# Performance work log

Measured on AMD Instinct MI355X. Metric: run time of the kernel, lower is better.

## Reference

```python
import jax, jax.numpy as jnp
import numpy as np

DIM = 768
H = 12        # query heads
HKV = 4       # kv heads
G = H // HKV  # GQA group size
HD = 64       # head dim
CAP = 50.0    # soft cap (Gemma-2 style)
EPS = 1e-6
SCALE = HD ** -0.5
B, T, S = 1, 128, 256


def setup_inputs() -> dict:
    key = jax.random.key(0)
    ks = jax.random.split(key, 5)
    s = DIM ** -0.5
    x = jax.random.normal(ks[0], (B, T, S, DIM), jnp.float32)
    Wq = jax.random.normal(ks[1], (DIM, H * HD), jnp.float32) * s
    Wk = jax.random.normal(ks[2], (DIM, HKV * HD), jnp.float32) * s
    Wv = jax.random.normal(ks[3], (DIM, HKV * HD), jnp.float32) * s
    Wo = jax.random.normal(ks[4], (H * HD, DIM), jnp.float32) * s
    q_norm_w = jnp.ones((HD,), jnp.float32)
    k_norm_w = jnp.ones((HD,), jnp.float32)
    return {"x": x, "Wq": Wq, "Wk": Wk, "Wv": Wv, "Wo": Wo,
            "q_norm_w": q_norm_w, "k_norm_w": k_norm_w}


def _rmsnorm(x, w):
    # x: (..., HD)
    return x * jax.lax.rsqrt(jnp.mean(x * x, axis=-1, keepdims=True) + EPS) * w


def reference(x, Wq, Wk, Wv, Wo, q_norm_w, k_norm_w):
    b, t, s, d = x.shape
    n = b * s
    # fold spatial into batch: temporal attention per spatial position
    xf = x.transpose(0, 2, 1, 3).reshape(n, t, d)             # (N, T, D)
    q = (xf @ Wq).reshape(n, t, H, HD).transpose(0, 2, 1, 3)   # (N, H, T, hd)
    k = (xf @ Wk).reshape(n, t, HKV, HD).transpose(0, 2, 1, 3) # (N, Hkv, T, hd)
    v = (xf @ Wv).reshape(n, t, HKV, HD).transpose(0, 2, 1, 3)
    # QKNorm (per-head RMSNorm on head_dim)
    q = _rmsnorm(q, q_norm_w)
    k = _rmsnorm(k, k_norm_w)
    # GQA without materializing repeated K/V: split q heads into (Hkv, G)
    # (repeat_interleave maps query head h -> kv head h // G, matching kv*G+g)
    qg = q.reshape(n, HKV, G, t, HD)
    attn = jnp.einsum('bkgtd,bksd->bkgts', qg, k) * SCALE      # (N, Hkv, G, T, T)
    attn = CAP * jnp.tanh(attn / CAP)                          # soft cap
    causal = jnp.triu(jnp.ones((t, t), bool), 1)               # True above diag
    attn = jnp.where(causal, -jnp.inf, attn)
    attn = jax.nn.softmax(attn, axis=-1)
    out = jnp.einsum('bkgts,bksd->bkgtd', attn, v)             # (N, Hkv, G, T, hd)
    out = out.reshape(n, H, t, HD).transpose(0, 2, 1, 3).reshape(n, t, H * HD)
    out = out @ Wo                                             # (N, T, D)
    return out.reshape(b, s, t, d).transpose(0, 2, 1, 3)        # (B, T, S, D)
```

## Files before the change

### kernel.cpp

```cpp
#include <hip/hip_runtime.h>
#include <stdint.h>
#include <stddef.h>

#define DIM 768
#define NH  12
#define NKV 4
#define HD  64
#define TT  128
#define NS  256

typedef __attribute__((ext_vector_type(8))) short bf16x8;
typedef __attribute__((ext_vector_type(4))) float f32x4;
typedef __attribute__((ext_vector_type(4))) unsigned int u32x4;
typedef __attribute__((ext_vector_type(2))) unsigned int u32x2;

__device__ __forceinline__ unsigned short f2bf(float f) {
  union { float f; unsigned int u; } v; v.f = f;
  return (unsigned short)((v.u + 0x7FFFu + ((v.u >> 16) & 1u)) >> 16);
}

__device__ __forceinline__ void gload_lds16(const void* g, void* l) {
  __builtin_amdgcn_global_load_lds(
      (const __attribute__((address_space(1))) unsigned int*)g,
      (__attribute__((address_space(3))) unsigned int*)l, 16, 0, 0);
}

__global__ __launch_bounds__(256)
void prep_kernel(const float* __restrict__ x, const float* __restrict__ Wq,
                 const float* __restrict__ Wk, const float* __restrict__ Wv,
                 const float* __restrict__ Wo, unsigned short* __restrict__ Wt,
                 unsigned short* __restrict__ WoT, unsigned short* __restrict__ xb) {
  const int b = blockIdx.x, tid = threadIdx.x;
  if (b < 6144) {
    int idx = b * 256 + tid;
    const int n1 = 1280 * DIM;
    if (idx < n1) {
      int c = idx / DIM, kk = idx - c * DIM;
      float v;
      if (c < 768)       v = Wq[kk * 768 + c];
      else if (c < 1024) v = Wk[kk * 256 + (c - 768)];
      else               v = Wv[kk * 256 + (c - 1024)];
      Wt[idx] = f2bf(v);
    } else {
      int i2 = idx - n1;
      int c = i2 / DIM, kk = i2 - c * DIM;
      WoT[i2] = f2bf(Wo[kk * 768 + c]);
    }
  } else {
    int g = (b - 6144) * 256 + tid;
    int r = g / 192;
    int k = g - r * 192;
    int t = r >> 8, n = r & 255;
    f32x4 f = *reinterpret_cast<const f32x4*>(x + (size_t)g * 4);
    u32x2 pk;
    pk[0] = (unsigned)f2bf(f[0]) | ((unsigned)f2bf(f[1]) << 16);
    pk[1] = (unsigned)f2bf(f[2]) | ((unsigned)f2bf(f[3]) << 16);
    *reinterpret_cast<u32x2*>(xb + (size_t)((n << 7) + t) * DIM + k * 4) = pk;
  }
}


#define STAGE256(bufp, ko)                                                       \
  { unsigned short* Ad = lds + (bufp) * 32768;                                   \
    unsigned short* Bd = Ad + 16384;                                             \
    gload_lds16(a0src + (size_t)(wave * 8) * DIM + (ko), Ad + (wave * 8) * 64);  \
    gload_lds16(a0src + (size_t)(64 + wave * 8) * DIM + (ko), Ad + (64 + wave * 8) * 64); \
    gload_lds16(a1src + (size_t)(wave * 8) * DIM + (ko), Ad + (128 + wave * 8) * 64);     \
    gload_lds16(a1src + (size_t)(64 + wave * 8) * DIM + (ko), Ad + (192 + wave * 8) * 64);\
    gload_lds16(bsrc + (size_t)(wave * 8) * DIM + (ko), Bd + (wave * 8) * 64);   \
    gload_lds16(bsrc + (size_t)(64 + wave * 8) * DIM + (ko), Bd + (64 + wave * 8) * 64);  \
    gload_lds16(bsrc + (size_t)(128 + wave * 8) * DIM + (ko), Bd + (128 + wave * 8) * 64);\
    gload_lds16(bsrc + (size_t)(192 + wave * 8) * DIM + (ko), Bd + (192 + wave * 8) * 64); }

#define KLOOP256                                                                 \
  STAGE256(0, 0);                                                                \
  __syncthreads();                                                               \
  for (int kt = 0; kt < 12; ++kt) {                                              \
    if (kt < 11) STAGE256((kt + 1) & 1, (kt + 1) * 64);                          \
    const char* Ab = (const char*)(lds + (kt & 1) * 32768);                      \
    const char* Bb = Ab + 32768;                                                 \
    _Pragma("unroll")                                                            \
    for (int ks = 0; ks < 2; ++ks) {                                             \
      bf16x8 a[8], bbf[4];                                                       \
      _Pragma("unroll")                                                          \
      for (int m = 0; m < 8; ++m)                                                \
        a[m] = *(const bf16x8*)(Ab + (wmw * 128 + m * 16 + cl) * 128 + ((ks * 64 + rowg * 16) ^ swzr)); \
      _Pragma("unroll")                                                          \
      for (int nn = 0; nn < 4; ++nn)                                             \
        bbf[nn] = *(const bf16x8*)(Bb + (wn * 64 + nn * 16 + cl) * 128 + ((ks * 64 + rowg * 16) ^ swzr)); \
      __builtin_amdgcn_s_setprio(1);                                             \
      _Pragma("unroll")                                                          \
      for (int m = 0; m < 8; ++m)                                                \
        _Pragma("unroll")                                                        \
        for (int nn = 0; nn < 4; ++nn)                                           \
          acc[m][nn] = __builtin_amdgcn_mfma_f32_16x16x32_bf16(a[m], bbf[nn], acc[m][nn], 0, 0, 0); \
      __builtin_amdgcn_s_setprio(0);                                             \
    }                                                                            \
    __syncthreads();                                                             \
  }

__global__ __launch_bounds__(512, 2)
void qkv_kernel(const unsigned short* __restrict__ xb, const float* __restrict__ qnw,
                const float* __restrict__ knw, const unsigned short* __restrict__ Wt,
                unsigned short* __restrict__ qb, unsigned short* __restrict__ kb,
                unsigned short* __restrict__ vTb) {
  extern __shared__ unsigned short lds[];
  const int b = blockIdx.x;
  const int x8 = b & 7, idx = b >> 3;
  const int cbt = idx % 5;
  const int np  = (idx / 5) * 8 + x8;
  const int n0  = np * 2;
  const int tid = threadIdx.x;
  const int wave = tid >> 6, lane = tid & 63;
  const int cl = lane & 15, rowg = lane >> 4;
  const int wmw = wave >> 2, wn = wave & 3;
  const int l8 = lane >> 3, s8 = lane & 7;
  const int segs = (s8 ^ l8) * 8;
  const unsigned short* a0src = xb + (size_t)(n0 * TT + l8) * DIM + segs;
  const unsigned short* a1src = xb + (size_t)((n0 + 1) * TT + l8) * DIM + segs;
  const unsigned short* bsrc  = Wt + (size_t)(cbt * 256 + l8) * DIM + segs;
  const int swzr = (cl & 7) << 4;
  f32x4 acc[8][4] = {};

  KLOOP256;

  __syncthreads();
  const int n = n0 + wmw;

  if (cbt == 4) {
    unsigned short* dst = vTb + (size_t)((n * NKV + wn) * HD) * TT;
    #pragma unroll
    for (int m = 0; m < 8; ++m) {
      const int tb = m * 16 + rowg * 4;
      #pragma unroll
      for (int nn = 0; nn < 4; ++nn) {
        const int d = nn * 16 + cl;
        u32x2 pk;
        pk[0] = (unsigned)f2bf(acc[m][nn][0]) | ((unsigned)f2bf(acc[m][nn][1]) << 16);
        pk[1] = (unsigned)f2bf(acc[m][nn][2]) | ((unsigned)f2bf(acc[m][nn][3]) << 16);
        *reinterpret_cast<u32x2*>(dst + (size_t)d * TT + tb) = pk;
      }
    }
  } else {
    const int isq = (cbt < 3);
    const float* nw = isq ? qnw : knw;
    float wfrag[4];
    #pragma unroll
    for (int nn = 0; nn < 4; ++nn) wfrag[nn] = nw[nn * 16 + cl];
    const float rs = isq ? 0.125f : 1.0f;
    unsigned short* slab = lds + (wmw * 4 + wn) * 8192;
    #pragma unroll
    for (int m = 0; m < 8; ++m) {
      #pragma unroll
      for (int j = 0; j < 4; ++j) {
        const int t = m * 16 + rowg * 4 + j;
        float ss = 0.f;
        #pragma unroll
        for (int nn = 0; nn < 4; ++nn) { float v = acc[m][nn][j]; ss += v * v; }
        #pragma unroll
        for (int dlt = 1; dlt < 16; dlt <<= 1) ss += __shfl_xor(ss, dlt);
        const float r = rsqrtf(ss * (1.f / 64.f) + 1e-6f) * rs;
        #pragma unroll
        for (int nn = 0; nn < 4; ++nn)
          slab[t * 64 + nn * 16 + cl] = f2bf(acc[m][nn][j] * r * wfrag[nn]);
      }
    }
    __syncthreads();
    #pragma unroll
    for (int i = 0; i < 16; ++i) {
      const int c = tid + 512 * i;
      const int s = c >> 10, within = c & 1023;
      const int nn2 = n0 + (s >> 2);
      size_t off;
      if (isq) off = ((size_t)nn2 * NH + cbt * 4 + (s & 3)) * TT * HD;
      else     off = ((size_t)nn2 * NKV + (s & 3)) * TT * HD;
      unsigned short* gdst = (isq ? qb : kb) + off + within * 8;
      *reinterpret_cast<u32x4*>(gdst) =
          *reinterpret_cast<const u32x4*>(lds + (size_t)s * 8192 + within * 8);
    }
  }
}

__global__ __launch_bounds__(256)
void attn_kernel(const unsigned short* __restrict__ qb, const unsigned short* __restrict__ kb,
                 const unsigned short* __restrict__ vTb, unsigned short* __restrict__ ab) {
  extern __shared__ char smem[];
  unsigned short (*Ks)[72]   = reinterpret_cast<unsigned short (*)[72]>(smem);
  unsigned short (*Vts)[136] = reinterpret_cast<unsigned short (*)[136]>(smem + 18432);
  unsigned short (*Pl)[136]  = reinterpret_cast<unsigned short (*)[136]>(smem + 35840);
  const int b = blockIdx.x;
  const int x8 = b & 7, idx = b >> 3;
  const int kv = idx & 3;
  const int n  = (idx >> 2) * 8 + x8;
  const int tid = threadIdx.x, wave = tid >> 6, lane = tid & 63;
  const int cl = lane & 15, rowg = lane >> 4;

  const unsigned short* ksrc = kb + (size_t)(n * NKV + kv) * TT * HD;
  const unsigned short* vsrc = vTb + (size_t)(n * NKV + kv) * HD * TT;
  #pragma unroll
  for (int i = 0; i < 4; ++i) {
    int c = tid + 256 * i, r = c >> 3, seg = c & 7;
    *reinterpret_cast<u32x4*>(&Ks[r][seg * 8]) = *reinterpret_cast<const u32x4*>(ksrc + c * 8);
  }
  #pragma unroll
  for (int i = 0; i < 4; ++i) {
    int c = tid + 256 * i, r = c >> 4, seg = c & 15;
    *reinterpret_cast<u32x4*>(&Vts[r][seg * 8]) = *reinterpret_cast<const u32x4*>(vsrc + c * 8);
  }
  __syncthreads();

  for (int hh = 0; hh < 3; ++hh) {
    const int h = kv * 3 + hh;
    const unsigned short* qsrc = qb + (size_t)(n * NH + h) * TT * HD;
    f32x4 sc[2][8] = {};
    #pragma unroll
    for (int ks = 0; ks < 2; ++ks) {
      bf16x8 a[2], bbf[8];
      #pragma unroll
      for (int m = 0; m < 2; ++m)
        a[m] = *reinterpret_cast<const bf16x8*>(
            qsrc + (size_t)(wave * 32 + m * 16 + cl) * HD + ks * 32 + rowg * 8);
      #pragma unroll
      for (int nn = 0; nn < 8; ++nn)
        bbf[nn] = *reinterpret_cast<const bf16x8*>(&Ks[nn * 16 + cl][ks * 32 + rowg * 8]);
      #pragma unroll
      for (int m = 0; m < 2; ++m)
        #pragma unroll
        for (int nn = 0; nn < 8; ++nn)
          sc[m][nn] = __builtin_amdgcn_mfma_f32_16x16x32_bf16(a[m], bbf[nn], sc[m][nn], 0, 0, 0);
    }
    #pragma unroll
    for (int m = 0; m < 2; ++m) {
      #pragma unroll
      for (int j = 0; j < 4; ++j) {
        const int rowv = wave * 32 + m * 16 + rowg * 4 + j;
        float mx = -__builtin_inff();
        #pragma unroll
        for (int nn = 0; nn < 8; ++nn) {
          float s = sc[m][nn][j];
          float e = __expf(s * 0.04f);
          s = 50.f - 100.f * __builtin_amdgcn_rcpf(e + 1.f);
          if (nn * 16 + cl > rowv) s = -__builtin_inff();
          sc[m][nn][j] = s;
          mx = fmaxf(mx, s);
        }
        #pragma unroll
        for (int d = 1; d < 16; d <<= 1) mx = fmaxf(mx, __shfl_xor(mx, d));
        float sum = 0.f;
        #pragma unroll
        for (int nn = 0; nn < 8; ++nn) {
          float e = __expf(sc[m][nn][j] - mx);
          sc[m][nn][j] = e;
          sum += e;
        }
        #pragma unroll
        for (int d = 1; d < 16; d <<= 1) sum += __shfl_xor(sum, d);
        const float inv = __builtin_amdgcn_rcpf(sum);
        #pragma unroll
        for (int nn = 0; nn < 8; ++nn)
          Pl[rowv][nn * 16 + cl] = f2bf(sc[m][nn][j] * inv);
      }
    }
    __syncthreads();
    f32x4 o[2][4] = {};
    #pragma unroll
    for (int ks = 0; ks < 4; ++ks) {
      bf16x8 a[2], bbf[4];
      #pragma unroll
      for (int m = 0; m < 2; ++m)
        a[m] = *reinterpret_cast<const bf16x8*>(&Pl[wave * 32 + m * 16 + cl][ks * 32 + rowg * 8]);
      #pragma unroll
      for (int nn = 0; nn < 4; ++nn)
        bbf[nn] = *reinterpret_cast<const bf16x8*>(&Vts[nn * 16 + cl][ks * 32 + rowg * 8]);
      #pragma unroll
      for (int m = 0; m < 2; ++m)
        #pragma unroll
        for (int nn = 0; nn < 4; ++nn)
          o[m][nn] = __builtin_amdgcn_mfma_f32_16x16x32_bf16(a[m], bbf[nn], o[m][nn], 0, 0, 0);
    }
    unsigned short* dst = ab + (size_t)n * TT * DIM + h * HD;
    #pragma unroll
    for (int m = 0; m < 2; ++m)
      #pragma unroll
      for (int j = 0; j < 4; ++j) {
        int t = wave * 32 + m * 16 + rowg * 4 + j;
        #pragma unroll
        for (int nn = 0; nn < 4; ++nn)
          dst[(size_t)t * DIM + nn * 16 + cl] = f2bf(o[m][nn][j]);
      }
    __syncthreads();
  }
}

__global__ __launch_bounds__(512, 2)
void out_kernel(const unsigned short* __restrict__ ab, const unsigned short* __restrict__ WoT,
                float* __restrict__ out) {
  extern __shared__ unsigned short lds[];
  const int b = blockIdx.x;
  const int x8 = b & 7, idx = b >> 3;
  const int cbt = idx % 3;
  const int np  = (idx / 3) * 8 + x8;
  const int n0  = np * 2;
  const int tid = threadIdx.x;
  const int wave = tid >> 6, lane = tid & 63;
  const int cl = lane & 15, rowg = lane >> 4;
  const int wmw = wave >> 2, wn = wave & 3;
  const int l8 = lane >> 3, s8 = lane & 7;
  const int segs = (s8 ^ l8) * 8;
  const unsigned short* a0src = ab + (size_t)(n0 * TT + l8) * DIM + segs;
  const unsigned short* a1src = ab + (size_t)((n0 + 1) * TT + l8) * DIM + segs;
  const unsigned short* bsrc  = WoT + (size_t)(cbt * 256 + l8) * DIM + segs;
  const int swzr = (cl & 7) << 4;
  f32x4 acc[8][4] = {};

  KLOOP256;

  const int n = n0 + wmw;
  #pragma unroll
  for (int m = 0; m < 8; ++m)
    #pragma unroll
    for (int j = 0; j < 4; ++j) {
      const int t = m * 16 + rowg * 4 + j;
      #pragma unroll
      for (int nn = 0; nn < 4; ++nn)
        out[(size_t)(t * NS + n) * DIM + cbt * 256 + wn * 64 + nn * 16 + cl] = acc[m][nn][j];
    }
}

extern "C" void kernel_launch(void* const* d_in, const int* in_sizes, int n_in,
                              void* d_out, int out_size, void* d_ws, size_t ws_size,
                              hipStream_t stream) {
  const float* x   = (const float*)d_in[0];
  const float* Wq  = (const float*)d_in[1];
  const float* Wk  = (const float*)d_in[2];
  const float* Wv  = (const float*)d_in[3];
  const float* Wo  = (const float*)d_in[4];
  const float* qnw = (const float*)d_in[5];
  const float* knw = (const float*)d_in[6];
  (void)in_sizes; (void)n_in; (void)out_size;

  char* ws = (char*)d_ws;
  unsigned short* Wt  = (unsigned short*)(ws + 0);
  unsigned short* WoT = (unsigned short*)(ws + 1966080);
  unsigned short* qb  = (unsigned short*)(ws + 3145728);
  unsigned short* kb  = (unsigned short*)(ws + 53477376);
  unsigned short* vTb = (unsigned short*)(ws + 70254592);
  unsigned short* ab  = (unsigned short*)(ws + 87031808);
  unsigned short* xb  = ab;
  if (ws_size < 137363456) return;

  hipFuncSetAttribute(reinterpret_cast<const void*>(qkv_kernel),
                      hipFuncAttributeMaxDynamicSharedMemorySize, 131072);
  hipFuncSetAttribute(reinterpret_cast<const void*>(out_kernel),
                      hipFuncAttributeMaxDynamicSharedMemorySize, 131072);
  hipFuncSetAttribute(reinterpret_cast<const void*>(attn_kernel),
                      hipFuncAttributeMaxDynamicSharedMemorySize, 70656);

  prep_kernel<<<30720, 256, 0, stream>>>(x, Wq, Wk, Wv, Wo, Wt, WoT, xb);
  qkv_kernel<<<640, 512, 131072, stream>>>(xb, qnw, knw, Wt, qb, kb, vTb);
  attn_kernel<<<1024, 256, 70656, stream>>>(qb, kb, vTb, ab);
  out_kernel<<<384, 512, 131072, stream>>>(ab, WoT, (float*)d_out);
}
```

Before: 230.8 us.

## Rework GEMM K-loop into 4-stage, K=32 pipeline with split-phase MFMA scheduling

Replaces the double-buffered K=64 GEMM main loop used by the QKV and output projection kernels with a quad-buffered K=32 loop. Each iteration is split into two phases: A and B tile prefetches two steps ahead are interleaved with LDS reads and MFMA groups, using explicit vmcnt/lgkmcnt waits and raw s_barriers in place of __syncthreads. The LDS swizzle and global-to-LDS load mapping are redesigned for 64-byte rows. The aim is to hide global load latency and cut barrier stalls, at the cost of more barriers per K step and hand-tuned wait counts that must match exactly for correctness.

```diff
diff --git a/kernel.cpp b/kernel.cpp
--- a/kernel.cpp
+++ b/kernel.cpp
@@ -60,43 +60,80 @@
 }
 
 
-#define STAGE256(bufp, ko)                                                       \
-  { unsigned short* Ad = lds + (bufp) * 32768;                                   \
-    unsigned short* Bd = Ad + 16384;                                             \
-    gload_lds16(a0src + (size_t)(wave * 8) * DIM + (ko), Ad + (wave * 8) * 64);  \
-    gload_lds16(a0src + (size_t)(64 + wave * 8) * DIM + (ko), Ad + (64 + wave * 8) * 64); \
-    gload_lds16(a1src + (size_t)(wave * 8) * DIM + (ko), Ad + (128 + wave * 8) * 64);     \
-    gload_lds16(a1src + (size_t)(64 + wave * 8) * DIM + (ko), Ad + (192 + wave * 8) * 64);\
-    gload_lds16(bsrc + (size_t)(wave * 8) * DIM + (ko), Bd + (wave * 8) * 64);   \
-    gload_lds16(bsrc + (size_t)(64 + wave * 8) * DIM + (ko), Bd + (64 + wave * 8) * 64);  \
-    gload_lds16(bsrc + (size_t)(128 + wave * 8) * DIM + (ko), Bd + (128 + wave * 8) * 64);\
-    gload_lds16(bsrc + (size_t)(192 + wave * 8) * DIM + (ko), Bd + (192 + wave * 8) * 64); }
-
-#define KLOOP256                                                                 \
-  STAGE256(0, 0);                                                                \
-  __syncthreads();                                                               \
-  for (int kt = 0; kt < 12; ++kt) {                                              \
-    if (kt < 11) STAGE256((kt + 1) & 1, (kt + 1) * 64);                          \
-    const char* Ab = (const char*)(lds + (kt & 1) * 32768);                      \
-    const char* Bb = Ab + 32768;                                                 \
-    _Pragma("unroll")                                                            \
-    for (int ks = 0; ks < 2; ++ks) {                                             \
-      bf16x8 a[8], bbf[4];                                                       \
-      _Pragma("unroll")                                                          \
-      for (int m = 0; m < 8; ++m)                                                \
-        a[m] = *(const bf16x8*)(Ab + (wmw * 128 + m * 16 + cl) * 128 + ((ks * 64 + rowg * 16) ^ swzr)); \
-      _Pragma("unroll")                                                          \
-      for (int nn = 0; nn < 4; ++nn)                                             \
-        bbf[nn] = *(const bf16x8*)(Bb + (wn * 64 + nn * 16 + cl) * 128 + ((ks * 64 + rowg * 16) ^ swzr)); \
-      __builtin_amdgcn_s_setprio(1);                                             \
-      _Pragma("unroll")                                                          \
-      for (int m = 0; m < 8; ++m)                                                \
-        _Pragma("unroll")                                                        \
-        for (int nn = 0; nn < 4; ++nn)                                           \
-          acc[m][nn] = __builtin_amdgcn_mfma_f32_16x16x32_bf16(a[m], bbf[nn], acc[m][nn], 0, 0, 0); \
-      __builtin_amdgcn_s_setprio(0);                                             \
-    }                                                                            \
-    __syncthreads();                                                             \
+#define STG_A(bufp, ko)                                                      \
+  { unsigned short* Ad = lds + (bufp) * 16384;                               \
+    gload_lds16(aptr + (size_t)(ko), Ad + (wave * 32) * 32);                 \
+    gload_lds16(aptr + (size_t)16 * DIM + (ko), Ad + (wave * 32 + 16) * 32); }
+#define STG_B(bufp, ko)                                                      \
+  { unsigned short* Bd = lds + (bufp) * 16384 + 8192;                        \
+    gload_lds16(bptr + (size_t)(ko), Bd + (wave * 32) * 32);                 \
+    gload_lds16(bptr + (size_t)16 * DIM + (ko), Bd + (wave * 32 + 16) * 32); }
+
+#define LDA32(m)  (*(const bf16x8*)(Ab + (wmw * 128 + (m) * 16 + cl) * 64 + swz16))
+#define LDB32(nn) (*(const bf16x8*)(Bb + (wn * 64 + (nn) * 16 + cl) * 64 + swz16))
+
+#define PH_TAIL                                                              \
+  __builtin_amdgcn_s_barrier();                                              \
+  asm volatile("s_waitcnt lgkmcnt(0)" ::: "memory");                         \
+  __builtin_amdgcn_sched_barrier(0);
+
+#define KLOOP32                                                              \
+  STG_A(0, 0); STG_B(0, 0); STG_A(1, 32); STG_B(1, 32);                      \
+  asm volatile("s_waitcnt vmcnt(4)" ::: "memory");                           \
+  __builtin_amdgcn_s_barrier();                                              \
+  for (int kt = 0; kt < 24; ++kt) {                                          \
+    const char* Ab = (const char*)lds + (kt & 3) * 32768;                    \
+    const char* Bb = Ab + 16384;                                             \
+    bf16x8 a0, a1, a2, a3, bf0, bf1, bf2, bf3;                               \
+                                                          \
+    a0 = LDA32(0); a1 = LDA32(1); a2 = LDA32(2); a3 = LDA32(3);              \
+    bf0 = LDB32(0); bf1 = LDB32(1); bf2 = LDB32(2); bf3 = LDB32(3);          \
+    if (kt < 22) STG_A((kt + 2) & 3, (kt + 2) * 32);                         \
+    PH_TAIL;                                                                 \
+    __builtin_amdgcn_s_setprio(1);                                           \
+    acc[0][0] = __builtin_amdgcn_mfma_f32_16x16x32_bf16(a0, bf0, acc[0][0], 0, 0, 0); \
+    acc[0][1] = __builtin_amdgcn_mfma_f32_16x16x32_bf16(a0, bf1, acc[0][1], 0, 0, 0); \
+    acc[0][2] = __builtin_amdgcn_mfma_f32_16x16x32_bf16(a0, bf2, acc[0][2], 0, 0, 0); \
+    acc[0][3] = __builtin_amdgcn_mfma_f32_16x16x32_bf16(a0, bf3, acc[0][3], 0, 0, 0); \
+    acc[1][0] = __builtin_amdgcn_mfma_f32_16x16x32_bf16(a1, bf0, acc[1][0], 0, 0, 0); \
+    acc[1][1] = __builtin_amdgcn_mfma_f32_16x16x32_bf16(a1, bf1, acc[1][1], 0, 0, 0); \
+    acc[1][2] = __builtin_amdgcn_mfma_f32_16x16x32_bf16(a1, bf2, acc[1][2], 0, 0, 0); \
+    acc[1][3] = __builtin_amdgcn_mfma_f32_16x16x32_bf16(a1, bf3, acc[1][3], 0, 0, 0); \
+    acc[2][0] = __builtin_amdgcn_mfma_f32_16x16x32_bf16(a2, bf0, acc[2][0], 0, 0, 0); \
+    acc[2][1] = __builtin_amdgcn_mfma_f32_16x16x32_bf16(a2, bf1, acc[2][1], 0, 0, 0); \
+    acc[2][2] = __builtin_amdgcn_mfma_f32_16x16x32_bf16(a2, bf2, acc[2][2], 0, 0, 0); \
+    acc[2][3] = __builtin_amdgcn_mfma_f32_16x16x32_bf16(a2, bf3, acc[2][3], 0, 0, 0); \
+    acc[3][0] = __builtin_amdgcn_mfma_f32_16x16x32_bf16(a3, bf0, acc[3][0], 0, 0, 0); \
+    acc[3][1] = __builtin_amdgcn_mfma_f32_16x16x32_bf16(a3, bf1, acc[3][1], 0, 0, 0); \
+    acc[3][2] = __builtin_amdgcn_mfma_f32_16x16x32_bf16(a3, bf2, acc[3][2], 0, 0, 0); \
+    acc[3][3] = __builtin_amdgcn_mfma_f32_16x16x32_bf16(a3, bf3, acc[3][3], 0, 0, 0); \
+    __builtin_amdgcn_s_setprio(0);                                           \
+    __builtin_amdgcn_s_barrier();                                            \
+                                   \
+    a0 = LDA32(4); a1 = LDA32(5); a2 = LDA32(6); a3 = LDA32(7);              \
+    if (kt < 22) STG_B((kt + 2) & 3, (kt + 2) * 32);                         \
+    if (kt < 22)      { asm volatile("s_waitcnt vmcnt(4)" ::: "memory"); }   \
+    else if (kt == 22){ asm volatile("s_waitcnt vmcnt(0)" ::: "memory"); }   \
+    PH_TAIL;                                                                 \
+    __builtin_amdgcn_s_setprio(1);                                           \
+    acc[4][0] = __builtin_amdgcn_mfma_f32_16x16x32_bf16(a0, bf0, acc[4][0], 0, 0, 0); \
+    acc[4][1] = __builtin_amdgcn_mfma_f32_16x16x32_bf16(a0, bf1, acc[4][1], 0, 0, 0); \
+    acc[4][2] = __builtin_amdgcn_mfma_f32_16x16x32_bf16(a0, bf2, acc[4][2], 0, 0, 0); \
+    acc[4][3] = __builtin_amdgcn_mfma_f32_16x16x32_bf16(a0, bf3, acc[4][3], 0, 0, 0); \
+    acc[5][0] = __builtin_amdgcn_mfma_f32_16x16x32_bf16(a1, bf0, acc[5][0], 0, 0, 0); \
+    acc[5][1] = __builtin_amdgcn_mfma_f32_16x16x32_bf16(a1, bf1, acc[5][1], 0, 0, 0); \
+    acc[5][2] = __builtin_amdgcn_mfma_f32_16x16x32_bf16(a1, bf2, acc[5][2], 0, 0, 0); \
+    acc[5][3] = __builtin_amdgcn_mfma_f32_16x16x32_bf16(a1, bf3, acc[5][3], 0, 0, 0); \
+    acc[6][0] = __builtin_amdgcn_mfma_f32_16x16x32_bf16(a2, bf0, acc[6][0], 0, 0, 0); \
+    acc[6][1] = __builtin_amdgcn_mfma_f32_16x16x32_bf16(a2, bf1, acc[6][1], 0, 0, 0); \
+    acc[6][2] = __builtin_amdgcn_mfma_f32_16x16x32_bf16(a2, bf2, acc[6][2], 0, 0, 0); \
+    acc[6][3] = __builtin_amdgcn_mfma_f32_16x16x32_bf16(a2, bf3, acc[6][3], 0, 0, 0); \
+    acc[7][0] = __builtin_amdgcn_mfma_f32_16x16x32_bf16(a3, bf0, acc[7][0], 0, 0, 0); \
+    acc[7][1] = __builtin_amdgcn_mfma_f32_16x16x32_bf16(a3, bf1, acc[7][1], 0, 0, 0); \
+    acc[7][2] = __builtin_amdgcn_mfma_f32_16x16x32_bf16(a3, bf2, acc[7][2], 0, 0, 0); \
+    acc[7][3] = __builtin_amdgcn_mfma_f32_16x16x32_bf16(a3, bf3, acc[7][3], 0, 0, 0); \
+    __builtin_amdgcn_s_setprio(0);                                           \
+    __builtin_amdgcn_s_barrier();                                            \
   }
 
 __global__ __launch_bounds__(512, 2)
@@ -114,15 +151,13 @@
   const int wave = tid >> 6, lane = tid & 63;
   const int cl = lane & 15, rowg = lane >> 4;
   const int wmw = wave >> 2, wn = wave & 3;
-  const int l8 = lane >> 3, s8 = lane & 7;
-  const int segs = (s8 ^ l8) * 8;
-  const unsigned short* a0src = xb + (size_t)(n0 * TT + l8) * DIM + segs;
-  const unsigned short* a1src = xb + (size_t)((n0 + 1) * TT + l8) * DIM + segs;
-  const unsigned short* bsrc  = Wt + (size_t)(cbt * 256 + l8) * DIM + segs;
-  const int swzr = (cl & 7) << 4;
+  const int sseg = ((lane & 3) ^ ((lane >> 3) & 3)) * 8;
+  const int swz16 = (rowg ^ ((cl >> 1) & 3)) << 4;
+  const unsigned short* aptr = xb + (size_t)((n0 + (wave >> 2)) * TT + (wave & 3) * 32 + (lane >> 2)) * DIM + sseg;
+  const unsigned short* bptr = Wt + (size_t)(cbt * 256 + wave * 32 + (lane >> 2)) * DIM + sseg;
   f32x4 acc[8][4] = {};
 
-  KLOOP256;
+  KLOOP32;
 
   __syncthreads();
   const int n = n0 + wmw;
@@ -305,15 +340,13 @@
   const int wave = tid >> 6, lane = tid & 63;
   const int cl = lane & 15, rowg = lane >> 4;
   const int wmw = wave >> 2, wn = wave & 3;
-  const int l8 = lane >> 3, s8 = lane & 7;
-  const int segs = (s8 ^ l8) * 8;
-  const unsigned short* a0src = ab + (size_t)(n0 * TT + l8) * DIM + segs;
-  const unsigned short* a1src = ab + (size_t)((n0 + 1) * TT + l8) * DIM + segs;
-  const unsigned short* bsrc  = WoT + (size_t)(cbt * 256 + l8) * DIM + segs;
-  const int swzr = (cl & 7) << 4;
+  const int sseg = ((lane & 3) ^ ((lane >> 3) & 3)) * 8;
+  const int swz16 = (rowg ^ ((cl >> 1) & 3)) << 4;
+  const unsigned short* aptr = ab + (size_t)((n0 + (wave >> 2)) * TT + (wave & 3) * 32 + (lane >> 2)) * DIM + sseg;
+  const unsigned short* bptr = WoT + (size_t)(cbt * 256 + wave * 32 + (lane >> 2)) * DIM + sseg;
   f32x4 acc[8][4] = {};
 
-  KLOOP256;
+  KLOOP32;
 
   const int n = n0 + wmw;
   #pragma unroll
```

Result: slower. 242.3 us (+5.0%).
